# Kernel tuning notes

Hardware: AMD Instinct MI355X
Metric: run time of the kernel (lower is better)

## Reference

```python
import jax, jax.numpy as jnp
import numpy as np

H, W = 85, 85
N_HEAD = 8

def layernorm(x, g, b, eps=1e-5):
    m = x.mean(-1, keepdims=True)
    v = ((x - m) ** 2).mean(-1, keepdims=True)
    return (x - m) * jax.lax.rsqrt(v + eps) * g + b


def setup_inputs() -> dict:
    key = jax.random.key(0)
    ks = jax.random.split(key, 12)
    B, C = 8, 256
    N = H * W
    hd = C // N_HEAD
    Ch = C * 4  # mlp_ratio = 4
    init = lambda k, fan_in, sh: (jax.random.normal(k, sh, jnp.float32) / np.float32(np.sqrt(fan_in)))
    d = {}
    d['fx'] = jax.random.normal(ks[0], (B, N, C), jnp.float32)
    # ln_1
    d['ln1_g'] = jnp.ones((C,), jnp.float32); d['ln1_b'] = jnp.zeros((C,), jnp.float32)
    # Galerkin linear attention projections (per-head split of C)
    d['Wq'] = init(ks[1], C, (C, C)); d['bq'] = jnp.zeros((C,), jnp.float32)
    d['Wk'] = init(ks[2], C, (C, C)); d['bk'] = jnp.zeros((C,), jnp.float32)
    d['Wv'] = init(ks[3], C, (C, C)); d['bv'] = jnp.zeros((C,), jnp.float32)
    d['Wo'] = init(ks[4], C, (C, C)); d['bo'] = jnp.zeros((C,), jnp.float32)
    # per-head LayerNorms on K and V (Galerkin normalization replacing softmax)
    d['kln_g'] = jnp.ones((N_HEAD, hd), jnp.float32); d['kln_b'] = jnp.zeros((N_HEAD, hd), jnp.float32)
    d['vln_g'] = jnp.ones((N_HEAD, hd), jnp.float32); d['vln_b'] = jnp.zeros((N_HEAD, hd), jnp.float32)
    # ln_2
    d['ln2_g'] = jnp.ones((C,), jnp.float32); d['ln2_b'] = jnp.zeros((C,), jnp.float32)
    # MLP (n_layers=0, res=False): pre linear + gelu, post linear
    d['W1'] = init(ks[5], C, (C, Ch)); d['b1'] = jnp.zeros((Ch,), jnp.float32)
    d['W2'] = init(ks[6], Ch, (Ch, C)); d['b2'] = jnp.zeros((C,), jnp.float32)
    return d


def reference(fx, ln1_g, ln1_b, Wq, bq, Wk, bk, Wv, bv, Wo, bo,
              kln_g, kln_b, vln_g, vln_b, ln2_g, ln2_b, W1, b1, W2, b2):
    B, N, C = fx.shape
    hd = C // N_HEAD
    x = layernorm(fx, ln1_g, ln1_b)  # [B,N,C]
    # (permute/reshape to image grid and back is a no-op for per-token attention math)
    split = lambda t: t.reshape(B, N, N_HEAD, hd).transpose(0, 2, 1, 3)  # [B,h,N,d]
    q = split(x @ Wq + bq)
    k = split(x @ Wk + bk)
    v = split(x @ Wv + bv)
    # Galerkin: LayerNorm on K and V over head dim, no softmax
    k = layernorm(k, kln_g[None, :, None, :], kln_b[None, :, None, :])
    v = layernorm(v, vln_g[None, :, None, :], vln_b[None, :, None, :])
    kv = jnp.einsum('bhnd,bhne->bhde', k, v) / N  # [B,h,d,d]
    attn = jnp.einsum('bhnd,bhde->bhne', q, kv)   # [B,h,N,d]
    attn = attn.transpose(0, 2, 1, 3).reshape(B, N, C)
    attn = attn @ Wo + bo
    fx = fx + attn  # residual 1
    x2 = layernorm(fx, ln2_g, ln2_b)
    x2 = jax.nn.gelu(x2 @ W1 + b1) @ W2 + b2
    return fx + x2  # residual 2
```

## Files before the change

kernel.cpp:

```cpp
#include <hip/hip_runtime.h>
#include <hip/hip_bf16.h>
#include <stdint.h>

#define B_ 8
#define NTOK 7225
#define MTOT (B_*NTOK)
#define MROWS 58368
#define MT_FULL 226
#define MT_BATCH 29

typedef unsigned short u16;
typedef u16 u16x8 __attribute__((ext_vector_type(8)));
typedef u16 u16x4 __attribute__((ext_vector_type(4)));
typedef __bf16 bf16x8 __attribute__((ext_vector_type(8)));
typedef float f32x4 __attribute__((ext_vector_type(4)));

__device__ inline float bf2f(u16 u){ union{float f;uint32_t i;}c; c.i=((uint32_t)u)<<16; return c.f; }
__device__ inline u16 f2bf(float f){ union{float f;uint32_t i;}c; c.f=f; uint32_t x=c.i;
                                     return (u16)((x + 0x7fffu + ((x>>16)&1u))>>16); }
__device__ inline uint32_t cvt_pk_bf16(float a, float b){
  uint32_t r; asm("v_cvt_pk_bf16_f32 %0, %1, %2" : "=v"(r) : "v"(a), "v"(b)); return r;
}
__device__ inline float gelu_f(float x){
  float t = 0.7978845608028654f * x * (1.0f + 0.044715f*x*x);
  float e = __expf(2.0f*t);
  return x * (1.0f - __builtin_amdgcn_rcpf(e + 1.0f));
}

__device__ inline void gload_lds16(const u16* g, u16* l) {
  __builtin_amdgcn_global_load_lds(
      (__attribute__((address_space(1))) void*)(const_cast<u16*>(g)),
      (__attribute__((address_space(3))) void*)(l), 16, 0, 0);
}

template<int EPI>
__global__ __launch_bounds__(512, 2)
void gemm256(const u16* __restrict__ A, int lda,
             const u16* __restrict__ Bm, int ldb, long bStride,
             const float* __restrict__ bias, int biasStride,
             const float* __restrict__ res,
             void* __restrict__ outp, int ldo,
             int K, int rowsValid, int batchRowStride,
             const float* __restrict__ g2, const float* __restrict__ b2,
             u16* __restrict__ x2out)
{
  __shared__ alignas(16) u16 lds[65536];
  const int tid = threadIdx.x;
  const int wid = tid >> 6, lane = tid & 63;
  const int wm = wid >> 2, wn = wid & 3;

  const int gx = gridDim.x, gy = gridDim.y;
  const int n = gx * gy;
  const int flat = blockIdx.y * gx + blockIdx.x;
  const int qq = n >> 3, rr = n & 7;
  const int xcd = flat & 7, pos = flat >> 3;
  const int swz = (xcd < rr ? xcd*(qq+1) : rr*(qq+1) + (xcd-rr)*qq) + pos;
  const int bx = swz / gy, by = swz % gy;
  const int bz = blockIdx.z;

  const long rowBase = (long)bz * batchRowStride + (long)bx * 256;
  const int colBase = by * 256;
  const u16* Bp = Bm + (long)bz * bStride;
  const float* biasP = bias + bz * biasStride;

  const int srow = lane >> 2;
  const int scol = ((lane & 3) ^ ((lane >> 3) & 3)) * 8;
  const int NT = K >> 6;

  auto stageHalf = [&](int bf, int kt, int sel) {
    const int sub = sel >> 1;
    const int k0 = (kt << 6) + sub*32 + scol;
    u16* base = lds + ((sel & 1) ? 32768 : 0) + (bf*2 + sub)*8192;
#pragma unroll
    for (int i = 0; i < 2; ++i) {
      const int r0 = (wid*2 + i)*16;
      if ((sel & 1) == 0)
        gload_lds16(A + (rowBase + r0 + srow)*(long)lda + k0, base + r0*32);
      else
        gload_lds16(Bp + (long)(colBase + r0 + srow)*ldb + k0, base + r0*32);
    }
  };

  f32x4 acc[8][4] = {};
  bf16x8 afr[4], bfr[4];
  const int lr = lane & 15;
  const int sl = lane >> 4;
  const int sp = (sl ^ ((lr >> 1) & 3)) * 8;

  stageHalf(0, 0, 0); stageHalf(0, 0, 1); stageHalf(0, 0, 2); stageHalf(0, 0, 3);

  for (int kt = 0; kt < NT; ++kt) {
    const int bf = kt & 1;
    const bool st = (kt + 1 < NT);
#pragma unroll
    for (int ph = 0; ph < 4; ++ph) {
      const int sub = ph >> 1, mh = ph & 1;
      if (ph == 0) {
        asm volatile("s_waitcnt vmcnt(4)" ::: "memory");
      } else if (ph == 2) {
        if (kt == NT - 1) asm volatile("s_waitcnt vmcnt(0)" ::: "memory");
        else              asm volatile("s_waitcnt vmcnt(4)" ::: "memory");
      } else {
        asm volatile("s_waitcnt vmcnt(6)" ::: "memory");
      }
      __builtin_amdgcn_s_barrier();
      const u16* Ab = lds + (bf*2 + sub)*8192;
      const u16* Bb = lds + 32768 + (bf*2 + sub)*8192;
      if (mh == 0) {
#pragma unroll
        for (int ni = 0; ni < 4; ++ni)
          bfr[ni] = *reinterpret_cast<const bf16x8*>(&Bb[(wn*64 + ni*16 + lr)*32 + sp]);
      }
#pragma unroll
      for (int i = 0; i < 4; ++i)
        afr[i] = *reinterpret_cast<const bf16x8*>(&Ab[(wm*128 + (mh*4 + i)*16 + lr)*32 + sp]);
      if (st) stageHalf(bf ^ 1, kt + 1, ph);
      asm volatile("s_waitcnt lgkmcnt(0)" ::: "memory");
      __builtin_amdgcn_sched_barrier(0);
      __builtin_amdgcn_s_setprio(1);
#pragma unroll
      for (int i = 0; i < 4; ++i)
#pragma unroll
        for (int ni = 0; ni < 4; ++ni)
          acc[mh*4 + i][ni] =
              __builtin_amdgcn_mfma_f32_16x16x32_bf16(bfr[ni], afr[i], acc[mh*4 + i][ni], 0, 0, 0);
      __builtin_amdgcn_s_setprio(0);
    }
  }

  const int cq = sl * 4;
  if (EPI <= 1) {
    __syncthreads();
#pragma unroll
    for (int mi = 0; mi < 8; ++mi) {
      const int r = wm*128 + mi*16 + lr;
#pragma unroll
      for (int ni = 0; ni < 4; ++ni) {
        const int c = wn*64 + ni*16 + cq;
        f32x4 v = acc[mi][ni] + *reinterpret_cast<const f32x4*>(&biasP[colBase + c]);
        uint2 pk;
        if (EPI == 1) { pk.x = cvt_pk_bf16(gelu_f(v[0]), gelu_f(v[1]));
                        pk.y = cvt_pk_bf16(gelu_f(v[2]), gelu_f(v[3])); }
        else          { pk.x = cvt_pk_bf16(v[0], v[1]); pk.y = cvt_pk_bf16(v[2], v[3]); }
        const int unit = ((c >> 3) ^ (r & 7));
        *reinterpret_cast<uint2*>(lds + r*256 + unit*8 + (c & 7)) = pk;
      }
    }
    __syncthreads();
#pragma unroll
    for (int p = 0; p < 16; ++p) {
      const int idx = p*512 + tid;
      const int r = idx >> 5, u = idx & 31;
      const int phys = u ^ (r & 7);
      u16x8 val = *reinterpret_cast<const u16x8*>(lds + r*256 + phys*8);
      *reinterpret_cast<u16x8*>((u16*)outp + (rowBase + r)*(long)ldo + colBase + u*8) = val;
    }
  } else if (EPI == 2) {
#pragma unroll
    for (int mi = 0; mi < 8; ++mi) {
      const int r = wm*128 + mi*16 + lr;
      if (bx*256 + r < rowsValid) {
        const long grow = rowBase + r;
#pragma unroll
        for (int ni = 0; ni < 4; ++ni) {
          const int c0 = colBase + wn*64 + ni*16 + cq;
          const long oidx = grow*(long)ldo + c0;
          f32x4 v = acc[mi][ni] + *reinterpret_cast<const f32x4*>(&biasP[c0]);
          f32x4 rv = *reinterpret_cast<const f32x4*>((const float*)res + oidx);
          *reinterpret_cast<f32x4*>((float*)outp + oidx) = v + rv;
        }
      }
    }
  } else {
    float* red = reinterpret_cast<float*>(lds);
    __syncthreads();
#pragma unroll
    for (int mi = 0; mi < 8; ++mi) {
      const int r = wm*128 + mi*16 + lr;
      const bool valid = (bx*256 + r < rowsValid);
      const long grow = rowBase + r;
      float s_r = 0.f, q_r = 0.f;
#pragma unroll
      for (int ni = 0; ni < 4; ++ni) {
        const int c0 = wn*64 + ni*16 + cq;
        f32x4 rv = valid ? *reinterpret_cast<const f32x4*>((const float*)res + grow*256 + c0)
                         : f32x4{0.f,0.f,0.f,0.f};
        f32x4 v = acc[mi][ni] + *reinterpret_cast<const f32x4*>(&biasP[c0]) + rv;
        acc[mi][ni] = v;
        s_r += v[0]+v[1]+v[2]+v[3];
        q_r += v[0]*v[0]+v[1]*v[1]+v[2]*v[2]+v[3]*v[3];
      }
      s_r += __shfl_xor(s_r, 16); s_r += __shfl_xor(s_r, 32);
      q_r += __shfl_xor(q_r, 16); q_r += __shfl_xor(q_r, 32);
      if (sl == 0) {
        red[       (wm*4 + wn)*128 + mi*16 + lr] = s_r;
        red[1024 + (wm*4 + wn)*128 + mi*16 + lr] = q_r;
      }
    }
    __syncthreads();
#pragma unroll
    for (int mi = 0; mi < 8; ++mi) {
      const int r = wm*128 + mi*16 + lr;
      if (bx*256 + r >= rowsValid) continue;
      const long grow = rowBase + r;
      const int rb = wm*4*128 + mi*16 + lr;
      float s_t = red[rb] + red[rb+128] + red[rb+256] + red[rb+384];
      float q_t = red[1024+rb] + red[1024+rb+128] + red[1024+rb+256] + red[1024+rb+384];
      const float m = s_t * (1.0f/256.0f);
      const float var = q_t * (1.0f/256.0f) - m*m;
      const float rs = rsqrtf(var + 1e-5f);
#pragma unroll
      for (int ni = 0; ni < 4; ++ni) {
        const int c0 = wn*64 + ni*16 + cq;
        const long oidx = grow*256 + c0;
        f32x4 v = acc[mi][ni];
        *reinterpret_cast<f32x4*>((float*)outp + oidx) = v;
        f32x4 gv = *reinterpret_cast<const f32x4*>(&g2[c0]);
        f32x4 bv = *reinterpret_cast<const f32x4*>(&b2[c0]);
        f32x4 xn = (v - m) * rs * gv + bv;
        uint2 pk; pk.x = cvt_pk_bf16(xn[0], xn[1]); pk.y = cvt_pk_bf16(xn[2], xn[3]);
        *reinterpret_cast<uint2*>(x2out + oidx) = pk;
      }
    }
  }
}

__global__ __launch_bounds__(256)
void ln_kernel(const float* __restrict__ in, const float* __restrict__ g,
               const float* __restrict__ bt, u16* __restrict__ out, int M)
{
  const int wv = threadIdx.x >> 6, lane = threadIdx.x & 63;
  const int t = blockIdx.x * 4 + wv;
  if (t >= M) return;
  const float4 x = reinterpret_cast<const float4*>(in + (long)t*256)[lane];
  float s = x.x + x.y + x.z + x.w;
  float q = x.x*x.x + x.y*x.y + x.z*x.z + x.w*x.w;
#pragma unroll
  for (int o = 32; o > 0; o >>= 1) { s += __shfl_xor(s, o); q += __shfl_xor(q, o); }
  const float m  = s * (1.0f/256.0f);
  const float var = q * (1.0f/256.0f) - m*m;
  const float rs = rsqrtf(var + 1e-5f);
  const float4 gv = reinterpret_cast<const float4*>(g)[lane];
  const float4 bv = reinterpret_cast<const float4*>(bt)[lane];
  uint2 o4;
  o4.x = cvt_pk_bf16((x.x - m)*rs*gv.x + bv.x, (x.y - m)*rs*gv.y + bv.y);
  o4.y = cvt_pk_bf16((x.z - m)*rs*gv.z + bv.z, (x.w - m)*rs*gv.w + bv.w);
  *reinterpret_cast<uint2*>(out + (long)t*256 + lane*4) = o4;
}

__global__ __launch_bounds__(256)
void kv_kernel(const u16* __restrict__ KV,
               const float* __restrict__ kg, const float* __restrict__ kb,
               const float* __restrict__ vg, const float* __restrict__ vb,
               float* __restrict__ kvout)
{
  const int bh = blockIdx.x, b = bh >> 3, h = bh & 7;
  const int tid = threadIdx.x;
  __shared__ u16 kls[256][32];
  __shared__ u16 vls[256][32];
  __shared__ float sg[4][32];
  if (tid < 32) {
    sg[0][tid] = kg[h*32 + tid];
    sg[1][tid] = kb[h*32 + tid];
    sg[2][tid] = vg[h*32 + tid];
    sg[3][tid] = vb[h*32 + tid];
  }
  const int d = tid >> 3, e0 = (tid & 7) * 4;
  float a0=0, a1=0, a2=0, a3=0;

  for (int sub = 0; sub < 2; ++sub) {
    const int r = blockIdx.y * 512 + sub * 256 + tid;
    __syncthreads();
    if (r < NTOK) {
      const u16* rowp = KV + (long)(b*NTOK + r)*512;
#pragma unroll
      for (int kv2 = 0; kv2 < 2; ++kv2) {
        const u16* p = rowp + (kv2 ? 256 : 0) + h*32;
        float xv[32]; float s = 0.f;
#pragma unroll
        for (int q4 = 0; q4 < 4; ++q4) {
          u16x8 u = *reinterpret_cast<const u16x8*>(p + q4*8);
#pragma unroll
          for (int j = 0; j < 8; ++j) { float f = bf2f(u[j]); xv[q4*8+j] = f; s += f; }
        }
        const float m = s * (1.0f/32.0f);
        float vv = 0.f;
#pragma unroll
        for (int j = 0; j < 32; ++j) { float d2 = xv[j]-m; vv += d2*d2; }
        const float rs = rsqrtf(vv*(1.0f/32.0f) + 1e-5f);
        const float* gg = sg[kv2 ? 2 : 0];
        const float* bb = sg[kv2 ? 3 : 1];
        u16 (*dst)[32] = kv2 ? vls : kls;
#pragma unroll
        for (int j = 0; j < 32; ++j) dst[tid][j] = f2bf((xv[j]-m)*rs*gg[j] + bb[j]);
      }
    } else {
#pragma unroll
      for (int j = 0; j < 32; ++j) { kls[tid][j] = 0; vls[tid][j] = 0; }
    }
    __syncthreads();
#pragma unroll 4
    for (int rr = 0; rr < 256; ++rr) {
      const float kd = bf2f(kls[rr][d]);
      u16x4 v4 = *reinterpret_cast<const u16x4*>(&vls[rr][e0]);
      a0 += kd * bf2f(v4[0]); a1 += kd * bf2f(v4[1]);
      a2 += kd * bf2f(v4[2]); a3 += kd * bf2f(v4[3]);
    }
  }
  const float sc = 1.0f / (float)NTOK;
  float* o = kvout + (long)bh*1024 + d*32 + e0;
  atomicAdd(o+0, a0*sc); atomicAdd(o+1, a1*sc);
  atomicAdd(o+2, a2*sc); atomicAdd(o+3, a3*sc);
}

__global__ __launch_bounds__(256)
void woeff_kernel(const float* __restrict__ kv, const float* __restrict__ Wo,
                  u16* __restrict__ Woet)
{
  const int b = blockIdx.x >> 8, c = blockIdx.x & 255;
  const int rtid = threadIdx.x;
  const int h = rtid >> 5, dd = rtid & 31;
  const float* kvp = kv + ((long)(b*8 + h)*32 + dd)*32;
  float s = 0.f;
#pragma unroll 8
  for (int e = 0; e < 32; ++e) s += kvp[e] * Wo[(h*32 + e)*256 + c];
  Woet[(long)(b*256 + c)*256 + rtid] = f2bf(s);
}

__global__ __launch_bounds__(256)
void watt_kernel(const u16* __restrict__ wq_bf, const u16* __restrict__ Woet,
                 u16* __restrict__ Watt)
{
  const int b = blockIdx.x >> 8, c = blockIdx.x & 255;
  const int k = threadIdx.x;
  const u16* wr = wq_bf + (long)k*256;
  const u16* er = Woet + ((long)(b*256 + c))*256;
  float s = 0.f;
#pragma unroll 4
  for (int j0 = 0; j0 < 256; j0 += 8) {
    u16x8 wv = *reinterpret_cast<const u16x8*>(wr + j0);
    u16x8 ev = *reinterpret_cast<const u16x8*>(er + j0);
#pragma unroll
    for (int j = 0; j < 8; ++j) s += bf2f(wv[j]) * bf2f(ev[j]);
  }
  Watt[((long)(b*256 + c))*256 + k] = f2bf(s);
}

__global__ __launch_bounds__(256)
void be_kernel(const float* __restrict__ bq, const float* __restrict__ bo,
               const u16* __restrict__ Woet, float* __restrict__ be)
{
  const int b = blockIdx.x, c = threadIdx.x;
  const u16* er = Woet + ((long)(b*256 + c))*256;
  float s = bo[c];
#pragma unroll 4
  for (int j0 = 0; j0 < 256; j0 += 8) {
    u16x8 ev = *reinterpret_cast<const u16x8*>(er + j0);
#pragma unroll
    for (int j = 0; j < 8; ++j) s += bq[j0+j] * bf2f(ev[j]);
  }
  be[b*256 + c] = s;
}

__device__ void transpose_tile(const float* __restrict__ src, u16* __restrict__ dst,
                               int R, int C, int tcx, int trY)
{
  __shared__ float t[32][33];
  const int tc = tcx * 32, tr = trY * 32;
  const int lx = threadIdx.x & 31, ly = threadIdx.x >> 5;
#pragma unroll
  for (int i = 0; i < 32; i += 8)
    t[ly + i][lx] = src[(long)(tr + ly + i)*C + tc + lx];
  __syncthreads();
#pragma unroll
  for (int i = 0; i < 32; i += 8)
    dst[(long)(tc + ly + i)*R + tr + lx] = f2bf(t[lx][ly + i]);
}

__global__ __launch_bounds__(256)
void prep_kernel(const float* __restrict__ Wk, const float* __restrict__ Wv,
                 const float* __restrict__ W1, const float* __restrict__ W2,
                 const float* __restrict__ Wq,
                 const float* __restrict__ bk, const float* __restrict__ bv,
                 u16* __restrict__ Wkv_t, u16* __restrict__ W1_t, u16* __restrict__ W2_t,
                 u16* __restrict__ wq_bf, float* __restrict__ kvb, float* __restrict__ bkv)
{
  int b = blockIdx.x;
  if (b < 256)      { transpose_tile(W1, W1_t, 256, 1024, b & 31, b >> 5); }
  else if (b < 512) { b -= 256; transpose_tile(W2, W2_t, 1024, 256, b & 7, b >> 3); }
  else if (b < 576) { b -= 512; transpose_tile(Wk, Wkv_t,         256, 256, b & 7, b >> 3); }
  else if (b < 640) { b -= 576; transpose_tile(Wv, Wkv_t + 65536, 256, 256, b & 7, b >> 3); }
  else if (b < 648) {
    const int base = (b - 640) * 8192 + threadIdx.x;
#pragma unroll
    for (int i = 0; i < 32; ++i) wq_bf[base + i*256] = f2bf(Wq[base + i*256]);
  } else if (b < 656) {
    const int base = (b - 648) * 8192 + threadIdx.x;
#pragma unroll
    for (int i = 0; i < 32; ++i) kvb[base + i*256] = 0.f;
  } else {
    const int i = threadIdx.x;
    bkv[i] = bk[i]; bkv[256 + i] = bv[i];
  }
}

extern "C" void kernel_launch(void* const* d_in, const int* in_sizes, int n_in,
                              void* d_out, int out_size, void* d_ws, size_t ws_size,
                              hipStream_t stream)
{
  const float* fx    = (const float*)d_in[0];
  const float* ln1_g = (const float*)d_in[1];
  const float* ln1_b = (const float*)d_in[2];
  const float* Wq = (const float*)d_in[3];
  const float* bq = (const float*)d_in[4];
  const float* Wk = (const float*)d_in[5];
  const float* bk = (const float*)d_in[6];
  const float* Wv = (const float*)d_in[7];
  const float* bv = (const float*)d_in[8];
  const float* Wo = (const float*)d_in[9];
  const float* bo = (const float*)d_in[10];
  const float* kg  = (const float*)d_in[11];
  const float* kbb = (const float*)d_in[12];
  const float* vg  = (const float*)d_in[13];
  const float* vbb = (const float*)d_in[14];
  const float* ln2_g = (const float*)d_in[15];
  const float* ln2_b = (const float*)d_in[16];
  const float* W1 = (const float*)d_in[17];
  const float* b1 = (const float*)d_in[18];
  const float* W2 = (const float*)d_in[19];
  const float* b2 = (const float*)d_in[20];
  float* outF = (float*)d_out;

  char* ws = (char*)d_ws;
  size_t off = 0;
  auto alloc = [&](size_t bytes) { char* p = ws + off; off += (bytes + 255) & ~(size_t)255; return p; };
  u16* bufX   = (u16*)alloc((size_t)MROWS*256*2);
  u16* bufKV  = (u16*)alloc((size_t)MROWS*512*2);
  u16* bufH   = (u16*)alloc((size_t)MROWS*1024*2);
  u16* Wkv_t  = (u16*)alloc(512*256*2);
  u16* W1_t   = (u16*)alloc(1024*256*2);
  u16* W2_t   = (u16*)alloc(256*1024*2);
  u16* Woe_t  = (u16*)alloc((size_t)8*256*256*2);
  u16* Watt   = (u16*)alloc((size_t)8*256*256*2);
  u16* wq_bf  = (u16*)alloc(256*256*2);
  float* kvb  = (float*)alloc((size_t)64*1024*4);
  float* bkv  = (float*)alloc(512*4);
  float* be   = (float*)alloc(8*256*4);
  (void)ws_size; (void)out_size; (void)n_in; (void)in_sizes;

  prep_kernel<<<657, 256, 0, stream>>>(Wk, Wv, W1, W2, Wq, bk, bv,
                                       Wkv_t, W1_t, W2_t, wq_bf, kvb, bkv);

  ln_kernel<<<MTOT/4, 256, 0, stream>>>(fx, ln1_g, ln1_b, bufX, MTOT);

  gemm256<0><<<dim3(MT_FULL, 2, 1), 512, 0, stream>>>(
      bufX, 256, Wkv_t, 256, 0, bkv, 0, nullptr, bufKV, 512, 256, MTOT, 0,
      nullptr, nullptr, nullptr);

  kv_kernel<<<dim3(64, 15), 256, 0, stream>>>(bufKV, kg, kbb, vg, vbb, kvb);

  woeff_kernel<<<2048, 256, 0, stream>>>(kvb, Wo, Woe_t);
  watt_kernel<<<2048, 256, 0, stream>>>(wq_bf, Woe_t, Watt);
  be_kernel<<<8, 256, 0, stream>>>(bq, bo, Woe_t, be);

  gemm256<3><<<dim3(MT_BATCH, 1, 8), 512, 0, stream>>>(
      bufX, 256, Watt, 256, 65536, be, 256, fx, outF, 256, 256, NTOK, NTOK,
      ln2_g, ln2_b, bufX);

  gemm256<1><<<dim3(MT_FULL, 4, 1), 512, 0, stream>>>(
      bufX, 256, W1_t, 256, 0, b1, 0, nullptr, bufH, 1024, 256, MTOT, 0,
      nullptr, nullptr, nullptr);

  gemm256<2><<<dim3(MT_FULL, 1, 1), 512, 0, stream>>>(
      bufH, 1024, W2_t, 1024, 0, b2, 0, outF, outF, 256, 1024, MTOT, 0,
      nullptr, nullptr, nullptr);
}
```

Before: 328.5 us.

## Add thin-K GEMM keeping weight slice resident in LDS for KV and W1 projections

Adds a gemm_thin kernel for the K=256 projections. Each block loads a 128-column weight slice into swizzled LDS once, then each wave streams 16-row A strips straight from global memory into registers and issues MFMAs against the resident weights, with an XCD-aware block remap. The KV projection and the W1+GELU projection now use this kernel instead of the double-buffered 256x256 tiled GEMM, and the now-unused EPI<=1 LDS-staged epilogue is removed. The aim is to drop the per-k-step staging and barriers. In exchange, A is re-read once per column block, and output stores are narrow, uncoalesced 8-byte writes.

Result: slower. 809.3 us (+146.4%).

```diff
diff --git a/kernel.cpp b/kernel.cpp
--- a/kernel.cpp
+++ b/kernel.cpp
@@ -6,6 +6,7 @@
 #define NTOK 7225
 #define MTOT (B_*NTOK)
 #define MROWS 58368
+#define NSTRIPS 3648
 #define MT_FULL 226
 #define MT_BATCH 29
 
@@ -31,6 +32,70 @@
   __builtin_amdgcn_global_load_lds(
       (__attribute__((address_space(1))) void*)(const_cast<u16*>(g)),
       (__attribute__((address_space(3))) void*)(l), 16, 0, 0);
+}
+
+template<int EPI>
+__global__ __launch_bounds__(512, 4)
+void gemm_thin(const u16* __restrict__ A, const u16* __restrict__ Bt,
+               const float* __restrict__ bias, u16* __restrict__ outp, int ldo)
+{
+  __shared__ alignas(16) u16 Bs[128][256];
+  const int tid = threadIdx.x;
+  const int wid = tid >> 6, lane = tid & 63;
+  const int lr = lane & 15, sl = lane >> 4;
+
+  const int mp = gridDim.y;
+  const int nfl = gridDim.x * mp;
+  const int flat = blockIdx.x * mp + blockIdx.y;
+  const int qq = nfl >> 3, rr = nfl & 7;
+  const int xcd = flat & 7, pos = flat >> 3;
+  const int swz = (xcd < rr ? xcd*(qq+1) : rr*(qq+1) + (xcd-rr)*qq) + pos;
+  const int nblk = swz / mp, mpart = swz % mp;
+
+  const u16* Bp = Bt + (long)nblk * 128 * 256;
+  const int nBase = nblk * 128;
+
+#pragma unroll
+  for (int i = 0; i < 8; ++i) {
+    const int j2 = (i*8 + wid) * 2;
+    const int row = j2 + (lane >> 5);
+    const int u = lane & 31;
+    const int gsl = (u ^ (row & 31)) << 3;
+    gload_lds16(Bp + row*256 + gsl, &Bs[j2][0]);
+  }
+  asm volatile("s_waitcnt vmcnt(0)" ::: "memory");
+  __builtin_amdgcn_s_barrier();
+
+  for (int s = mpart*8 + wid; s < NSTRIPS; s += mp*8) {
+    const long r0 = (long)s * 16;
+    const u16* Ap = A + (r0 + lr) * 256;
+    bf16x8 afr[8];
+#pragma unroll
+    for (int kk = 0; kk < 8; ++kk)
+      afr[kk] = *reinterpret_cast<const bf16x8*>(Ap + kk*32 + sl*8);
+    f32x4 acc[8] = {};
+#pragma unroll
+    for (int kk = 0; kk < 8; ++kk) {
+#pragma unroll
+      for (int ct = 0; ct < 8; ++ct) {
+        const int row = ct*16 + lr;
+        const int u = (kk*4 + sl) ^ (row & 31);
+        bf16x8 bfr = *reinterpret_cast<const bf16x8*>(&Bs[row][u*8]);
+        acc[ct] = __builtin_amdgcn_mfma_f32_16x16x32_bf16(bfr, afr[kk], acc[ct], 0, 0, 0);
+      }
+    }
+    u16* orow = outp + (r0 + lr)*(long)ldo + nBase;
+#pragma unroll
+    for (int ct = 0; ct < 8; ++ct) {
+      const int c = ct*16 + sl*4;
+      f32x4 v = acc[ct] + *reinterpret_cast<const f32x4*>(&bias[nBase + c]);
+      uint2 pk;
+      if (EPI == 1) { pk.x = cvt_pk_bf16(gelu_f(v[0]), gelu_f(v[1]));
+                      pk.y = cvt_pk_bf16(gelu_f(v[2]), gelu_f(v[3])); }
+      else          { pk.x = cvt_pk_bf16(v[0], v[1]); pk.y = cvt_pk_bf16(v[2], v[3]); }
+      *reinterpret_cast<uint2*>(orow + c) = pk;
+    }
+  }
 }
 
 template<int EPI>
@@ -129,33 +194,7 @@
   }
 
   const int cq = sl * 4;
-  if (EPI <= 1) {
-    __syncthreads();
-#pragma unroll
-    for (int mi = 0; mi < 8; ++mi) {
-      const int r = wm*128 + mi*16 + lr;
-#pragma unroll
-      for (int ni = 0; ni < 4; ++ni) {
-        const int c = wn*64 + ni*16 + cq;
-        f32x4 v = acc[mi][ni] + *reinterpret_cast<const f32x4*>(&biasP[colBase + c]);
-        uint2 pk;
-        if (EPI == 1) { pk.x = cvt_pk_bf16(gelu_f(v[0]), gelu_f(v[1]));
-                        pk.y = cvt_pk_bf16(gelu_f(v[2]), gelu_f(v[3])); }
-        else          { pk.x = cvt_pk_bf16(v[0], v[1]); pk.y = cvt_pk_bf16(v[2], v[3]); }
-        const int unit = ((c >> 3) ^ (r & 7));
-        *reinterpret_cast<uint2*>(lds + r*256 + unit*8 + (c & 7)) = pk;
-      }
-    }
-    __syncthreads();
-#pragma unroll
-    for (int p = 0; p < 16; ++p) {
-      const int idx = p*512 + tid;
-      const int r = idx >> 5, u = idx & 31;
-      const int phys = u ^ (r & 7);
-      u16x8 val = *reinterpret_cast<const u16x8*>(lds + r*256 + phys*8);
-      *reinterpret_cast<u16x8*>((u16*)outp + (rowBase + r)*(long)ldo + colBase + u*8) = val;
-    }
-  } else if (EPI == 2) {
+  if (EPI == 2) {
 #pragma unroll
     for (int mi = 0; mi < 8; ++mi) {
       const int r = wm*128 + mi*16 + lr;
@@ -453,9 +492,7 @@
 
   ln_kernel<<<MTOT/4, 256, 0, stream>>>(fx, ln1_g, ln1_b, bufX, MTOT);
 
-  gemm256<0><<<dim3(MT_FULL, 2, 1), 512, 0, stream>>>(
-      bufX, 256, Wkv_t, 256, 0, bkv, 0, nullptr, bufKV, 512, 256, MTOT, 0,
-      nullptr, nullptr, nullptr);
+  gemm_thin<0><<<dim3(4, 128), 512, 0, stream>>>(bufX, Wkv_t, bkv, bufKV, 512);
 
   kv_kernel<<<dim3(64, 15), 256, 0, stream>>>(bufKV, kg, kbb, vg, vbb, kvb);
 
@@ -467,9 +504,7 @@
       bufX, 256, Watt, 256, 65536, be, 256, fx, outF, 256, 256, NTOK, NTOK,
       ln2_g, ln2_b, bufX);
 
-  gemm256<1><<<dim3(MT_FULL, 4, 1), 512, 0, stream>>>(
-      bufX, 256, W1_t, 256, 0, b1, 0, nullptr, bufH, 1024, 256, MTOT, 0,
-      nullptr, nullptr, nullptr);
+  gemm_thin<1><<<dim3(8, 64), 512, 0, stream>>>(bufX, W1_t, b1, bufH, 1024);
 
   gemm256<2><<<dim3(MT_FULL, 1, 1), 512, 0, stream>>>(
       bufH, 1024, W2_t, 1024, 0, b2, 0, outF, outF, 256, 1024, MTOT, 0,
```

## Fuse MLP up and down projections into one kernel keeping hidden in LDS

Applied to the files above, without the earlier changes.

Replaces the two MLP GEMM launches with a single kernel. Each block processes 64 rows and loops over 128-wide hidden chunks: it computes the W1 chunk with GELU, stores it to LDS, and accumulates the W2 product into registers. This removes the write and read of the 58k×1024 bf16 hidden buffer in global memory. In exchange, each block must restream all of W1 and W2 from L2. The small 64-row tile with no double buffering, since every stage waits on vmcnt(0), may reduce MFMA utilization compared with the 256×256 tiled GEMMs.

After: 318.0 us. 1.03x faster.

```diff
diff --git a/kernel.cpp b/kernel.cpp
--- a/kernel.cpp
+++ b/kernel.cpp
@@ -8,6 +8,7 @@
 #define MROWS 58368
 #define MT_FULL 226
 #define MT_BATCH 29
+#define MLP_TILES 904
 
 typedef unsigned short u16;
 typedef u16 u16x8 __attribute__((ext_vector_type(8)));
@@ -155,22 +156,6 @@
       u16x8 val = *reinterpret_cast<const u16x8*>(lds + r*256 + phys*8);
       *reinterpret_cast<u16x8*>((u16*)outp + (rowBase + r)*(long)ldo + colBase + u*8) = val;
     }
-  } else if (EPI == 2) {
-#pragma unroll
-    for (int mi = 0; mi < 8; ++mi) {
-      const int r = wm*128 + mi*16 + lr;
-      if (bx*256 + r < rowsValid) {
-        const long grow = rowBase + r;
-#pragma unroll
-        for (int ni = 0; ni < 4; ++ni) {
-          const int c0 = colBase + wn*64 + ni*16 + cq;
-          const long oidx = grow*(long)ldo + c0;
-          f32x4 v = acc[mi][ni] + *reinterpret_cast<const f32x4*>(&biasP[c0]);
-          f32x4 rv = *reinterpret_cast<const f32x4*>((const float*)res + oidx);
-          *reinterpret_cast<f32x4*>((float*)outp + oidx) = v + rv;
-        }
-      }
-    }
   } else {
     float* red = reinterpret_cast<float*>(lds);
     __syncthreads();
@@ -221,6 +206,106 @@
         uint2 pk; pk.x = cvt_pk_bf16(xn[0], xn[1]); pk.y = cvt_pk_bf16(xn[2], xn[3]);
         *reinterpret_cast<uint2*>(x2out + oidx) = pk;
       }
+    }
+  }
+}
+
+__global__ __launch_bounds__(512, 1)
+void mlp_fused2(const u16* __restrict__ x2, const u16* __restrict__ W1t,
+                const u16* __restrict__ W2t, const float* __restrict__ b1,
+                const float* __restrict__ b2, float* __restrict__ outF,
+                int rowsValid)
+{
+  __shared__ alignas(16) u16 Xs[64*256];
+  __shared__ alignas(16) u16 Wsb[32768];
+  __shared__ alignas(16) u16 Hs[64*128];
+  const int tid = threadIdx.x;
+  const int wid = tid >> 6, lane = tid & 63;
+  const int wm = wid >> 1, wn = wid & 1;
+  const int lr = lane & 15, sl = lane >> 4;
+  const long rowBase = (long)blockIdx.x * 64;
+  const int rA = wm*16 + lr;
+
+#pragma unroll
+  for (int i = 0; i < 4; ++i) {
+    const int u = i*512 + tid;
+    const int r = u >> 5, pu = u & 31;
+    gload_lds16(x2 + (rowBase + r)*256 + ((pu ^ (r & 31)) << 3), &Xs[u*8]);
+  }
+  auto stageW1 = [&](int c) {
+#pragma unroll
+    for (int i = 0; i < 8; ++i) {
+      const int u = i*512 + tid;
+      const int r = u >> 5, pu = u & 31;
+      gload_lds16(W1t + (long)(c*128 + r)*256 + ((pu ^ (r & 31)) << 3), &Wsb[u*8]);
+    }
+  };
+  auto stageW2 = [&](int c) {
+#pragma unroll
+    for (int i = 0; i < 8; ++i) {
+      const int u = i*512 + tid;
+      const int r = u >> 4, pu = u & 15;
+      gload_lds16(W2t + (long)r*1024 + c*128 + ((pu ^ (r & 15)) << 3), &Wsb[u*8]);
+    }
+  };
+  stageW1(0);
+  asm volatile("s_waitcnt vmcnt(0)" ::: "memory");
+  __syncthreads();
+
+  f32x4 acc2[8] = {};
+  for (int c = 0; c < 8; ++c) {
+    f32x4 acc1[4] = {};
+#pragma unroll
+    for (int kk = 0; kk < 8; ++kk) {
+      const int u = kk*4 + sl;
+      bf16x8 xa = *reinterpret_cast<const bf16x8*>(&Xs[(rA*32 + (u ^ (rA & 31)))*8]);
+#pragma unroll
+      for (int ni = 0; ni < 4; ++ni) {
+        const int rB = wn*64 + ni*16 + lr;
+        bf16x8 wb = *reinterpret_cast<const bf16x8*>(&Wsb[(rB*32 + (u ^ (rB & 31)))*8]);
+        acc1[ni] = __builtin_amdgcn_mfma_f32_16x16x32_bf16(wb, xa, acc1[ni], 0, 0, 0);
+      }
+    }
+    __builtin_amdgcn_s_barrier();
+    stageW2(c);
+    const float* b1c = b1 + c*128;
+#pragma unroll
+    for (int ni = 0; ni < 4; ++ni) {
+      const int col = wn*64 + ni*16 + sl*4;
+      f32x4 v = acc1[ni] + *reinterpret_cast<const f32x4*>(&b1c[col]);
+      uint2 pk; pk.x = cvt_pk_bf16(gelu_f(v[0]), gelu_f(v[1]));
+      pk.y = cvt_pk_bf16(gelu_f(v[2]), gelu_f(v[3]));
+      const int uw = (col >> 3) ^ (rA & 15);
+      *reinterpret_cast<uint2*>(&Hs[rA*128 + uw*8 + (col & 7)]) = pk;
+    }
+    asm volatile("s_waitcnt vmcnt(0)" ::: "memory");
+    __syncthreads();
+#pragma unroll
+    for (int kk = 0; kk < 4; ++kk) {
+      const int u = kk*4 + sl;
+      bf16x8 ha = *reinterpret_cast<const bf16x8*>(&Hs[(rA*16 + (u ^ (rA & 15)))*8]);
+#pragma unroll
+      for (int nj = 0; nj < 8; ++nj) {
+        const int rB = wn*128 + nj*16 + lr;
+        bf16x8 wb = *reinterpret_cast<const bf16x8*>(&Wsb[(rB*16 + (u ^ (rB & 15)))*8]);
+        acc2[nj] = __builtin_amdgcn_mfma_f32_16x16x32_bf16(wb, ha, acc2[nj], 0, 0, 0);
+      }
+    }
+    __builtin_amdgcn_s_barrier();
+    if (c + 1 < 8) {
+      stageW1(c + 1);
+      asm volatile("s_waitcnt vmcnt(0)" ::: "memory");
+      __syncthreads();
+    }
+  }
+  if (rowBase + rA < rowsValid) {
+    float* orow = outF + (rowBase + rA)*256;
+#pragma unroll
+    for (int nj = 0; nj < 8; ++nj) {
+      const int col = wn*128 + nj*16 + sl*4;
+      f32x4 v = acc2[nj] + *reinterpret_cast<const f32x4*>(&b2[col])
+              + *reinterpret_cast<const f32x4*>(&orow[col]);
+      *reinterpret_cast<f32x4*>(&orow[col]) = v;
     }
   }
 }
@@ -436,7 +521,6 @@
   auto alloc = [&](size_t bytes) { char* p = ws + off; off += (bytes + 255) & ~(size_t)255; return p; };
   u16* bufX   = (u16*)alloc((size_t)MROWS*256*2);
   u16* bufKV  = (u16*)alloc((size_t)MROWS*512*2);
-  u16* bufH   = (u16*)alloc((size_t)MROWS*1024*2);
   u16* Wkv_t  = (u16*)alloc(512*256*2);
   u16* W1_t   = (u16*)alloc(1024*256*2);
   u16* W2_t   = (u16*)alloc(256*1024*2);
@@ -467,11 +551,5 @@
       bufX, 256, Watt, 256, 65536, be, 256, fx, outF, 256, 256, NTOK, NTOK,
       ln2_g, ln2_b, bufX);
 
-  gemm256<1><<<dim3(MT_FULL, 4, 1), 512, 0, stream>>>(
-      bufX, 256, W1_t, 256, 0, b1, 0, nullptr, bufH, 1024, 256, MTOT, 0,
-      nullptr, nullptr, nullptr);
-
-  gemm256<2><<<dim3(MT_FULL, 1, 1), 512, 0, stream>>>(
-      bufH, 1024, W2_t, 1024, 0, b2, 0, outF, outF, 256, 1024, MTOT, 0,
-      nullptr, nullptr, nullptr);
-}
+  mlp_fused2<<<MLP_TILES, 512, 0, stream>>>(bufX, W1_t, W2_t, b1, b2, outF, MTOT);
+}
```
